# Performance work log

Hardware: AMD Instinct MI355X
Metric: run time of the kernel (lower is better)

The kernel has to match this reference:

```python
import jax, jax.numpy as jnp
import numpy as np

B, T, H, W, L, E = 16384, 14, 16, 8, 26, 128  # words, letters/word, letter image, labels, embed


def setup_inputs() -> dict:
    key = jax.random.key(0)
    k1, k2, k3, k4 = jax.random.split(key, 4)
    X = jax.random.normal(k1, (B, T, E), jnp.float32)
    conv_w = jax.random.normal(k2, (1, 1, 5, 5), jnp.float32) * 0.1
    conv_b = jax.random.normal(k3, (1,), jnp.float32) * 0.1
    params = jax.random.normal(k4, (L * E + L * L,), jnp.float32) * 0.1
    return {"X": X, "conv_w": conv_w, "conv_b": conv_b, "params": params}


def _conv_features(X, conv_w, conv_b):
    # __reshape_before_conv__: (B,T,128) -> (B*T,1,16,8); Conv(5): single-channel 5x5 'same' conv
    x = X.reshape(B * T, 1, H, W)
    y = jax.lax.conv_general_dilated(
        x, conv_w, window_strides=(1, 1), padding="SAME",
        dimension_numbers=("NCHW", "OIHW", "NCHW"))
    y = y + conv_b[None, :, None, None]
    # __reshape_after_conv__: (B*T,1,16,8) -> (B,14,128)
    return y.reshape(B, T, H * W)


def reference(X, conv_w, conv_b, params):
    feats = _conv_features(X, conv_w, conv_b)          # [B,T,E]
    Wmat = params[: L * E].reshape(L, E)               # emission weights
    Trans = params[L * E:].reshape(L, L)               # Trans[prev,next]
    emis = jnp.einsum("bte,le->btl", feats, Wmat)      # node potentials [B,T,L]

    # Viterbi (max-sum) DP over the T=14 letters — dp_infer
    alpha0 = emis[:, 0]                                # [B,L]

    def step(alpha, e_t):
        scores = alpha[:, :, None] + Trans[None]       # [B,L_prev,L_next]
        bp = jnp.argmax(scores, axis=1)                # best previous label [B,L]
        alpha_new = jnp.max(scores, axis=1) + e_t
        return alpha_new, bp

    alpha_T, backptrs = jax.lax.scan(step, alpha0, jnp.swapaxes(emis[:, 1:], 0, 1))
    last = jnp.argmax(alpha_T, axis=1)                 # label at time T-1, [B]
    score = jnp.max(alpha_T, axis=1)                   # Viterbi max score, [B]

    # backtrack: reverse scan over backpointers
    def back(lbl, bp):
        prev = jnp.take_along_axis(bp, lbl[:, None], axis=1)[:, 0]
        return prev, lbl

    first, path_rest = jax.lax.scan(back, last, backptrs, reverse=True)
    # path_rest[t] = label at time t+1 (stacked in original order); first = label at time 0
    preds = jnp.concatenate([first[:, None], jnp.swapaxes(path_rest, 0, 1)], axis=1)  # [B,T]
    return preds.astype(jnp.int32), score
```

## Files before the change

### kernel.cpp

```cpp
#include <hip/hip_runtime.h>

#define TT 14
#define LL 26
#define EE 128
#define NB 16384
#define BPB 8
#define ROWS (BPB * TT)

__global__ __launch_bounds__(256) void crf_setup(
    const float* __restrict__ conv_w, const float* __restrict__ conv_b,
    const float* __restrict__ params, float* __restrict__ weff,
    float* __restrict__ be) {
  int idx = blockIdx.x * 256 + threadIdx.x;
  if (idx < EE * LL) {
    int e = idx / LL, l = idx - e * LL;
    int iy = e >> 3, ix = e & 7;
    float s = 0.f;
    for (int ky = 0; ky < 5; ++ky) {
      int oy = iy - ky + 2;
      if (oy < 0 || oy >= 16) continue;
      for (int kx = 0; kx < 5; ++kx) {
        int ox = ix - kx + 2;
        if (ox < 0 || ox >= 8) continue;
        s += conv_w[ky * 5 + kx] * params[l * EE + oy * 8 + ox];
      }
    }
    weff[e * LL + l] = s;
  }
  if (idx < LL) {
    float s = 0.f;
    for (int e = 0; e < EE; ++e) s += params[idx * EE + e];
    be[idx] = conv_b[0] * s;
  }
}

__global__ __launch_bounds__(128) void crf_main(
    const float* __restrict__ X, const float* __restrict__ params,
    const float* __restrict__ weff, const float* __restrict__ be,
    float* __restrict__ out) {
  __shared__ float emis_s[ROWS][28];
  __shared__ float Ts[LL * LL];
  __shared__ unsigned char bp_s[BPB][TT - 1][28];

  const int tid = threadIdx.x;
  const int b0 = blockIdx.x * BPB;

  for (int i = tid; i < LL * LL; i += 128) Ts[i] = params[LL * EE + i];

  if (tid < ROWS) {
    const float4* xv =
        reinterpret_cast<const float4*>(X) + (size_t)(b0 * TT + tid) * 32;
    float acc[LL];
#pragma unroll
    for (int l = 0; l < LL; ++l) acc[l] = 0.f;
    for (int e4 = 0; e4 < 32; ++e4) {
      float4 v = xv[e4];
      const float* w = weff + e4 * 4 * LL;
#pragma unroll
      for (int l = 0; l < LL; ++l)
        acc[l] += v.x * w[l] + v.y * w[LL + l] + v.z * w[2 * LL + l] +
                  v.w * w[3 * LL + l];
    }
#pragma unroll
    for (int l = 0; l < LL; ++l) emis_s[tid][l] = acc[l] + be[l];
  }
  __syncthreads();

  const int lane = tid & 63;
  const int wv = tid >> 6;
  const int j = lane & 31;
  const int hb = lane >> 5;
  const int jj = (j < LL) ? j : (LL - 1);

  for (int p = 0; p < 2; ++p) {
    const int bl = p * 4 + wv * 2 + hb;
    float Tcol[LL];
#pragma unroll
    for (int i = 0; i < LL; ++i) Tcol[i] = Ts[i * LL + jj];

    float alpha = emis_s[bl * TT + 0][jj];
    for (int t = 1; t < TT; ++t) {
      float m = -__builtin_inff();
      int bp = 0;
#pragma unroll
      for (int i = 0; i < LL; ++i) {
        float a_i = __shfl(alpha, i, 32);
        float s = a_i + Tcol[i];
        if (s > m) { m = s; bp = i; }
      }
      alpha = m + emis_s[bl * TT + t][jj];
      if (j < LL) bp_s[bl][t - 1][j] = (unsigned char)bp;
    }

    float val = (j < LL) ? alpha : -__builtin_inff();
    int idx = j;
#pragma unroll
    for (int off = 16; off >= 1; off >>= 1) {
      float v2 = __shfl_xor(val, off, 32);
      int i2 = __shfl_xor(idx, off, 32);
      if (v2 > val || (v2 == val && i2 < idx)) { val = v2; idx = i2; }
    }

    __syncthreads();

    if (j == 0) {
      const int b = b0 + bl;
      out[NB * TT + b] = val;
      int lbl = idx;
      for (int t = TT - 1; t >= 1; --t) {
        out[b * TT + t] = (float)lbl;
        lbl = bp_s[bl][t - 1][lbl];
      }
      out[b * TT + 0] = (float)lbl;
    }
    __syncthreads();
  }
}

extern "C" void kernel_launch(void* const* d_in, const int* in_sizes, int n_in,
                              void* d_out, int out_size, void* d_ws,
                              size_t ws_size, hipStream_t stream) {
  const float* X = (const float*)d_in[0];
  const float* conv_w = (const float*)d_in[1];
  const float* conv_b = (const float*)d_in[2];
  const float* params = (const float*)d_in[3];
  float* out = (float*)d_out;
  float* weff = (float*)d_ws;
  float* be = weff + EE * LL;

  hipLaunchKernelGGL(crf_setup, dim3(13), dim3(256), 0, stream, conv_w, conv_b,
                     params, weff, be);
  hipLaunchKernelGGL(crf_main, dim3(NB / BPB), dim3(128), 0, stream, X, params,
                     weff, be, out);
}
```

Measured before the change: 89.37 us.

## Stage X through LDS in coalesced chunks and coalesce output writes

The emission GEMV now loads X cooperatively in 16-element column chunks, with all threads issuing coalesced float4 loads into a padded shared buffer, instead of each thread striding through its own 512-byte row. Predictions and scores are staged in shared memory and written out by contiguous threads rather than by a single lane per word. Padding of the emission buffer changes to 27 to avoid bank conflicts, and launch bounds request 4 blocks per CU. The cost is extra barriers per chunk and reuse of shared memory between the X tile and the backpointers.

Result: slower. 123.7 us (+38.4%).

```diff
diff --git a/kernel.cpp b/kernel.cpp
--- a/kernel.cpp
+++ b/kernel.cpp
@@ -6,6 +6,9 @@
 #define NB 16384
 #define BPB 8
 #define ROWS (BPB * TT)
+#define CH 16
+#define XPAD 17
+#define EPAD 27
 
 __global__ __launch_bounds__(256) void crf_setup(
     const float* __restrict__ conv_w, const float* __restrict__ conv_b,
@@ -34,35 +37,53 @@
   }
 }
 
-__global__ __launch_bounds__(128) void crf_main(
+__global__ __launch_bounds__(128, 4) void crf_main(
     const float* __restrict__ X, const float* __restrict__ params,
     const float* __restrict__ weff, const float* __restrict__ be,
     float* __restrict__ out) {
-  __shared__ float emis_s[ROWS][28];
+  __shared__ float emis_s[ROWS * EPAD];
   __shared__ float Ts[LL * LL];
-  __shared__ unsigned char bp_s[BPB][TT - 1][28];
+  __shared__ float uni[ROWS * XPAD];
+  unsigned char* bp_s = (unsigned char*)uni;
+  float* preds_s = uni + (BPB * 13 * 28) / 4;
+  float* score_s = preds_s + ROWS;
 
   const int tid = threadIdx.x;
   const int b0 = blockIdx.x * BPB;
 
   for (int i = tid; i < LL * LL; i += 128) Ts[i] = params[LL * EE + i];
 
+  float acc[LL];
+#pragma unroll
+  for (int l = 0; l < LL; ++l) acc[l] = 0.f;
+  const float4* Xv = reinterpret_cast<const float4*>(X) + (size_t)b0 * TT * 32;
+
+  for (int c = 0; c < EE / CH; ++c) {
+    __syncthreads();
+#pragma unroll
+    for (int k = 0; k < 4; ++k) {
+      int fid = k * 128 + tid;
+      if (fid < ROWS * 4) {
+        int row = fid >> 2, q = fid & 3;
+        float4 v = Xv[row * 32 + c * 4 + q];
+        float* xp = &uni[row * XPAD + q * 4];
+        xp[0] = v.x; xp[1] = v.y; xp[2] = v.z; xp[3] = v.w;
+      }
+    }
+    __syncthreads();
+    if (tid < ROWS) {
+      const float* w = weff + c * CH * LL;
+#pragma unroll
+      for (int e = 0; e < CH; ++e) {
+        float xv = uni[tid * XPAD + e];
+#pragma unroll
+        for (int l = 0; l < LL; ++l) acc[l] += xv * w[e * LL + l];
+      }
+    }
+  }
   if (tid < ROWS) {
-    const float4* xv =
-        reinterpret_cast<const float4*>(X) + (size_t)(b0 * TT + tid) * 32;
-    float acc[LL];
 #pragma unroll
-    for (int l = 0; l < LL; ++l) acc[l] = 0.f;
-    for (int e4 = 0; e4 < 32; ++e4) {
-      float4 v = xv[e4];
-      const float* w = weff + e4 * 4 * LL;
-#pragma unroll
-      for (int l = 0; l < LL; ++l)
-        acc[l] += v.x * w[l] + v.y * w[LL + l] + v.z * w[2 * LL + l] +
-                  v.w * w[3 * LL + l];
-    }
-#pragma unroll
-    for (int l = 0; l < LL; ++l) emis_s[tid][l] = acc[l] + be[l];
+    for (int l = 0; l < LL; ++l) emis_s[tid * EPAD + l] = acc[l] + be[l];
   }
   __syncthreads();
 
@@ -78,7 +99,7 @@
 #pragma unroll
     for (int i = 0; i < LL; ++i) Tcol[i] = Ts[i * LL + jj];
 
-    float alpha = emis_s[bl * TT + 0][jj];
+    float alpha = emis_s[(bl * TT + 0) * EPAD + jj];
     for (int t = 1; t < TT; ++t) {
       float m = -__builtin_inff();
       int bp = 0;
@@ -88,8 +109,8 @@
         float s = a_i + Tcol[i];
         if (s > m) { m = s; bp = i; }
       }
-      alpha = m + emis_s[bl * TT + t][jj];
-      if (j < LL) bp_s[bl][t - 1][j] = (unsigned char)bp;
+      alpha = m + emis_s[(bl * TT + t) * EPAD + jj];
+      if (j < LL) bp_s[(bl * 13 + (t - 1)) * 28 + j] = (unsigned char)bp;
     }
 
     float val = (j < LL) ? alpha : -__builtin_inff();
@@ -104,16 +125,21 @@
     __syncthreads();
 
     if (j == 0) {
-      const int b = b0 + bl;
-      out[NB * TT + b] = val;
+      score_s[bl] = val;
       int lbl = idx;
       for (int t = TT - 1; t >= 1; --t) {
-        out[b * TT + t] = (float)lbl;
-        lbl = bp_s[bl][t - 1][lbl];
+        preds_s[bl * TT + t] = (float)lbl;
+        lbl = bp_s[(bl * 13 + (t - 1)) * 28 + lbl];
       }
-      out[b * TT + 0] = (float)lbl;
+      preds_s[bl * TT + 0] = (float)lbl;
     }
     __syncthreads();
+  }
+
+  if (tid < ROWS) {
+    out[(size_t)b0 * TT + tid] = preds_s[tid];
+  } else if (tid < ROWS + BPB) {
+    out[(size_t)NB * TT + b0 + (tid - ROWS)] = score_s[tid - ROWS];
   }
 }
 
```
